# Kernel optimization log

Measured on AMD Instinct MI355X. Metric: run time of the kernel, lower is better.

Reference implementation:

```python
import jax, jax.numpy as jnp
import numpy as np

N, M, D, DV = 16384, 16384, 8, 16
BLOCK = 2048  # row tile size; kernel block is [BLOCK, M], never materialize full [N, M]


def setup_inputs() -> dict:
    key = jax.random.key(0)
    k1, k2, k3, k4 = jax.random.split(key, 4)
    ls = jax.random.uniform(k1, (D,), dtype=jnp.float32)          # per-dim lengthscale weights (positive)
    x = jax.random.normal(k2, (N, D), dtype=jnp.float32)
    y = jax.random.normal(k3, (M, D), dtype=jnp.float32)
    b = jax.random.normal(k4, (M, DV), dtype=jnp.float32)
    return {"ls": ls, "x": x, "y": y, "b": b}


def reference(ls, x, y, b):
    # Matern nu=2.5 kernel-weighted reduction:
    #   d2_ij = sum_d ls_d * (x_id - y_jd)^2
    #   K_ij  = (1 + c1*sqrt(d2) + c2*d2) * exp(-c1*sqrt(d2))   (c1=sqrt(5), c2=sqrt(5/3), as in the torch module)
    #   out_i = sum_j K_ij * b_j   -- computed in row tiles (KeOps-style online reduction)
    c1 = jnp.sqrt(jnp.asarray(5.0, x.dtype))
    c2 = jnp.sqrt(jnp.asarray(5.0 / 3.0, x.dtype))

    def row_block(xi):  # xi: [BLOCK, D]
        diff = xi[:, None, :] - y[None, :, :]                 # [BLOCK, M, D]
        d2 = jnp.einsum('d,bmd->bm', ls, diff * diff)         # [BLOCK, M]
        r = jnp.sqrt(d2)
        k = (1.0 + c1 * r + c2 * d2) * jnp.exp(-c1 * r)       # [BLOCK, M]
        return k @ b                                          # [BLOCK, DV]

    xb = x.reshape(-1, BLOCK, x.shape[1])                     # [N/BLOCK, BLOCK, D]
    out = jax.lax.map(row_block, xb)                          # [N/BLOCK, BLOCK, DV]
    return out.reshape(-1, b.shape[1])                        # [N, DV]
```

## Files before the change

### kernel.cpp

```cpp
#include <hip/hip_runtime.h>
#include <stdint.h>

#define NN 16384
#define MM 16384
#define DD 8
#define DV 16
#define WAVES 4
#define MT 2
#define ROWS_WAVE (MT * 16)
#define ROWS_BLK (WAVES * ROWS_WAVE)
#define JSPLIT 32
#define JCHUNK (MM / JSPLIT)
#define J32 (JCHUNK / 32)

typedef short bf8 __attribute__((ext_vector_type(8)));
typedef short s2v __attribute__((ext_vector_type(2)));
typedef float f32x4 __attribute__((ext_vector_type(4)));

#define C3SQ 10.406844905028037f
#define C2S  (1.2909944487358056f / 10.406844905028037f)
#define LN2  0.6931471805599453f

__device__ __forceinline__ unsigned short f2bf(float f) {
    union { float f; uint32_t u; } c; c.f = f;
    uint32_t u = c.u + 0x7FFF + ((c.u >> 16) & 1);
    return (unsigned short)(u >> 16);
}
__device__ __forceinline__ float bf2f(unsigned short h) {
    union { float f; uint32_t u; } c; c.u = ((uint32_t)h) << 16;
    return c.f;
}

#define BF16_ONE ((short)0x3F80)

__global__ __launch_bounds__(256) void prep_frags(const float* __restrict__ ls,
                                                  const float* __restrict__ y,
                                                  const float* __restrict__ b,
                                                  bf8* __restrict__ ytbl,
                                                  bf8* __restrict__ btbl,
                                                  float4* __restrict__ outz) {
    const int tile = blockIdx.x * 4 + (threadIdx.x >> 6);
    const int lane = threadIdx.x & 63;
    const int n = lane & 15, quad = lane >> 4;

    outz[blockIdx.x * 256 + threadIdx.x] = make_float4(0.f, 0.f, 0.f, 0.f);

    float lsv[DD];
#pragma unroll
    for (int d = 0; d < DD; ++d) lsv[d] = ls[d];

    const float4* yr4 = (const float4*)(y + (size_t)(tile * 16 + n) * DD);
    float4 ya = yr4[0], yb = yr4[1];
    float yv[DD] = {ya.x, ya.y, ya.z, ya.w, yb.x, yb.y, yb.z, yb.w};

    float syv = 0.f;
    unsigned short wh[DD], wl[DD];
#pragma unroll
    for (int d = 0; d < DD; ++d) {
        syv = fmaf(lsv[d] * yv[d], yv[d], syv);
        float w = -2.f * C3SQ * yv[d];
        wh[d] = f2bf(w);
        wl[d] = f2bf(w - bf2f(wh[d]));
    }

    bf8 fr;
    if (quad < 3) {
#pragma unroll
        for (int d = 0; d < DD; ++d)
            fr[d] = (short)((quad == 2) ? wl[d] : wh[d]);
    } else {
        float csy = C3SQ * syv;
        unsigned short sh = f2bf(csy);
        unsigned short sl = f2bf(csy - bf2f(sh));
        fr[0] = (short)sh;
        fr[1] = (short)sl;
        fr[2] = BF16_ONE;
        fr[3] = BF16_ONE;
        fr[4] = 0; fr[5] = 0; fr[6] = 0; fr[7] = 0;
    }
    ytbl[tile * 64 + lane] = fr;

    if (tile < MM / 32) {
        bf8 bfr;
#pragma unroll
        for (int s = 0; s < 8; ++s) {
            int k = quad * 8 + s;
            int jl = (k >> 1) + ((k & 1) << 4);
            float bv = b[(size_t)(tile * 32 + jl) * DV + n];
            bfr[s] = (short)f2bf(bv);
        }
        btbl[tile * 64 + lane] = bfr;
    }
}

__global__ __launch_bounds__(256, 8) void matern_mfma(const float* __restrict__ ls,
                                                      const float* __restrict__ x,
                                                      const bf8* __restrict__ ytbl,
                                                      const bf8* __restrict__ btbl,
                                                      float* __restrict__ out) {
    const int t = threadIdx.x;
    const int lane = t & 63, wave = t >> 6;
    const int n = lane & 15, quad = lane >> 4;
    const int waverow = blockIdx.x * ROWS_BLK + wave * ROWS_WAVE;

    __shared__ __attribute__((aligned(16))) unsigned short klds[WAVES][MT][16][40];

    float lsv[DD];
#pragma unroll
    for (int d = 0; d < DD; ++d) lsv[d] = ls[d];

    bf8 afrag[MT];
#pragma unroll
    for (int mt = 0; mt < MT; ++mt) {
        const float* xr = x + (size_t)(waverow + mt * 16 + n) * DD;
        float sx = 0.f;
        unsigned short xh[DD], xl[DD];
#pragma unroll
        for (int d = 0; d < DD; ++d) {
            float xv = xr[d];
            float xlsv = lsv[d] * xv;
            sx = fmaf(xlsv, xv, sx);
            xh[d] = f2bf(xlsv);
            xl[d] = f2bf(xlsv - bf2f(xh[d]));
        }
        bf8 fr;
        if (quad == 3) {
            float csx = C3SQ * sx;
            unsigned short sh = f2bf(csx);
            unsigned short sl = f2bf(csx - bf2f(sh));
            fr[0] = BF16_ONE;
            fr[1] = BF16_ONE;
            fr[2] = (short)sh;
            fr[3] = (short)sl;
            fr[4] = 0; fr[5] = 0; fr[6] = 0; fr[7] = 0;
        } else {
#pragma unroll
            for (int d = 0; d < DD; ++d)
                fr[d] = (short)((quad == 1) ? xl[d] : xh[d]);
        }
        afrag[mt] = fr;
    }

    f32x4 acc[MT];
#pragma unroll
    for (int mt = 0; mt < MT; ++mt) acc[mt] = (f32x4){0.f, 0.f, 0.f, 0.f};

    const int tile16base = blockIdx.y * (JCHUNK / 16);
    const int tile32base = blockIdx.y * (JCHUNK / 32);

#pragma unroll 1
    for (int it = 0; it < J32; ++it) {
        const int tl0 = tile16base + it * 2;
        bf8 yA = ytbl[(size_t)tl0 * 64 + lane];
        bf8 yB = ytbl[(size_t)(tl0 + 1) * 64 + lane];
        bf8 bb = btbl[(size_t)(tile32base + it) * 64 + lane];

#pragma unroll
        for (int mt = 0; mt < MT; ++mt) {
            f32x4 z = (f32x4){0.f, 0.f, 0.f, 0.f};
            f32x4 s0 = __builtin_amdgcn_mfma_f32_16x16x32_bf16(afrag[mt], yA, z, 0, 0, 0);
            f32x4 s1 = __builtin_amdgcn_mfma_f32_16x16x32_bf16(afrag[mt], yB, z, 0, 0, 0);
#pragma unroll
            for (int s = 0; s < 4; ++s) {
                float a0 = __builtin_fabsf(s0[s]);
                float a1 = __builtin_fabsf(s1[s]);
                float t0 = __builtin_amdgcn_sqrtf(a0);
                float t1 = __builtin_amdgcn_sqrtf(a1);
                float e0 = __builtin_amdgcn_exp2f(-t0);
                float e1 = __builtin_amdgcn_exp2f(-t1);
                float k0 = fmaf(C2S, a0, fmaf(LN2, t0, 1.f)) * e0;
                float k1 = fmaf(C2S, a1, fmaf(LN2, t1, 1.f)) * e1;
                s2v w;
#if __has_builtin(__builtin_amdgcn_cvt_pk_bf16_f32)
                typedef __bf16 bf2v __attribute__((ext_vector_type(2)));
                bf2v pk = __builtin_amdgcn_cvt_pk_bf16_f32(k0, k1);
                union { bf2v v; s2v s; } cv; cv.v = pk;
                w = cv.s;
#else
                w[0] = (short)((__float_as_uint(k0) + 0x8000u) >> 16);
                w[1] = (short)((__float_as_uint(k1) + 0x8000u) >> 16);
#endif
                *(s2v*)&klds[wave][mt][quad * 4 + s][2 * n] = w;
            }
        }
#pragma unroll
        for (int mt = 0; mt < MT; ++mt) {
            const bf8* kp = (const bf8*)&klds[wave][mt][n][quad * 8];
            acc[mt] = __builtin_amdgcn_mfma_f32_16x16x32_bf16(*kp, bb, acc[mt], 0, 0, 0);
        }
    }

#pragma unroll
    for (int mt = 0; mt < MT; ++mt)
#pragma unroll
        for (int s = 0; s < 4; ++s) {
            const int row = waverow + mt * 16 + quad * 4 + s;
            atomicAdd(out + (size_t)row * DV + n, acc[mt][s]);
        }
}

extern "C" void kernel_launch(void* const* d_in, const int* in_sizes, int n_in,
                              void* d_out, int out_size, void* d_ws, size_t ws_size,
                              hipStream_t stream) {
    const float* ls = (const float*)d_in[0];
    const float* x  = (const float*)d_in[1];
    const float* y  = (const float*)d_in[2];
    const float* b  = (const float*)d_in[3];
    float* out = (float*)d_out;

    char* ws = (char*)d_ws;
    bf8* ytbl = (bf8*)ws;
    bf8* btbl = (bf8*)(ws + (1 << 20));

    prep_frags<<<MM / 64, 256, 0, stream>>>(ls, y, b, ytbl, btbl, (float4*)out);
    matern_mfma<<<dim3(NN / ROWS_BLK, JSPLIT), 256, 0, stream>>>(ls, x, ytbl, btbl, out);
}
```

Measured before the change: 136.2 us.

## Prefetch next tile fragments and pack Matern elementwise math into float2 ops

Loads the y and b fragments for the next j-tile one iteration ahead, so global load latency overlaps the current tile's MFMA and transcendental work. Rewrites the per-element kernel evaluation as two-wide float vectors so the compiler can emit packed FMA/mul instructions. Clamps to zero with max instead of fabs, and packs to bf16 with a single perm instead of the cvt builtin. Costs extra registers for the prefetched fragments, which may reduce occupancy. The final iteration issues one redundant wrapped-around load.

```diff
diff --git a/kernel.cpp b/kernel.cpp
--- a/kernel.cpp
+++ b/kernel.cpp
@@ -14,7 +14,7 @@
 #define J32 (JCHUNK / 32)
 
 typedef short bf8 __attribute__((ext_vector_type(8)));
-typedef short s2v __attribute__((ext_vector_type(2)));
+typedef float f32x2 __attribute__((ext_vector_type(2)));
 typedef float f32x4 __attribute__((ext_vector_type(4)));
 
 #define C3SQ 10.406844905028037f
@@ -148,39 +148,42 @@
     const int tile16base = blockIdx.y * (JCHUNK / 16);
     const int tile32base = blockIdx.y * (JCHUNK / 32);
 
+    const bf8* ybase = ytbl + (size_t)tile16base * 64 + lane;
+    const bf8* bbase = btbl + (size_t)tile32base * 64 + lane;
+
+    bf8 yA = ybase[0];
+    bf8 yB = ybase[64];
+    bf8 bb = bbase[0];
+
 #pragma unroll 1
     for (int it = 0; it < J32; ++it) {
-        const int tl0 = tile16base + it * 2;
-        bf8 yA = ytbl[(size_t)tl0 * 64 + lane];
-        bf8 yB = ytbl[(size_t)(tl0 + 1) * 64 + lane];
-        bf8 bb = btbl[(size_t)(tile32base + it) * 64 + lane];
+        const int nx = (it + 1) & (J32 - 1);
+        bf8 pyA = ybase[(size_t)nx * 128];
+        bf8 pyB = ybase[(size_t)nx * 128 + 64];
+        bf8 pbb = bbase[(size_t)nx * 64];
 
 #pragma unroll
         for (int mt = 0; mt < MT; ++mt) {
-            f32x4 z = (f32x4){0.f, 0.f, 0.f, 0.f};
-            f32x4 s0 = __builtin_amdgcn_mfma_f32_16x16x32_bf16(afrag[mt], yA, z, 0, 0, 0);
-            f32x4 s1 = __builtin_amdgcn_mfma_f32_16x16x32_bf16(afrag[mt], yB, z, 0, 0, 0);
+            f32x4 z4 = (f32x4){0.f, 0.f, 0.f, 0.f};
+            f32x4 s0 = __builtin_amdgcn_mfma_f32_16x16x32_bf16(afrag[mt], yA, z4, 0, 0, 0);
+            f32x4 s1 = __builtin_amdgcn_mfma_f32_16x16x32_bf16(afrag[mt], yB, z4, 0, 0, 0);
 #pragma unroll
             for (int s = 0; s < 4; ++s) {
-                float a0 = __builtin_fabsf(s0[s]);
-                float a1 = __builtin_fabsf(s1[s]);
-                float t0 = __builtin_amdgcn_sqrtf(a0);
-                float t1 = __builtin_amdgcn_sqrtf(a1);
-                float e0 = __builtin_amdgcn_exp2f(-t0);
-                float e1 = __builtin_amdgcn_exp2f(-t1);
-                float k0 = fmaf(C2S, a0, fmaf(LN2, t0, 1.f)) * e0;
-                float k1 = fmaf(C2S, a1, fmaf(LN2, t1, 1.f)) * e1;
-                s2v w;
-#if __has_builtin(__builtin_amdgcn_cvt_pk_bf16_f32)
-                typedef __bf16 bf2v __attribute__((ext_vector_type(2)));
-                bf2v pk = __builtin_amdgcn_cvt_pk_bf16_f32(k0, k1);
-                union { bf2v v; s2v s; } cv; cv.v = pk;
-                w = cv.s;
-#else
-                w[0] = (short)((__float_as_uint(k0) + 0x8000u) >> 16);
-                w[1] = (short)((__float_as_uint(k1) + 0x8000u) >> 16);
-#endif
-                *(s2v*)&klds[wave][mt][quad * 4 + s][2 * n] = w;
+                f32x2 a = {s0[s], s1[s]};
+                a = __builtin_elementwise_max(a, (f32x2){0.f, 0.f});
+                f32x2 tt = {__builtin_amdgcn_sqrtf(a[0]),
+                            __builtin_amdgcn_sqrtf(a[1])};
+                f32x2 ee = {__builtin_amdgcn_exp2f(-tt[0]),
+                            __builtin_amdgcn_exp2f(-tt[1])};
+                f32x2 pp = __builtin_elementwise_fma(
+                               (f32x2){C2S, C2S}, a,
+                               __builtin_elementwise_fma((f32x2){LN2, LN2}, tt,
+                                                         (f32x2){1.f, 1.f}));
+                f32x2 kk = pp * ee;
+                unsigned int u0 = __float_as_uint(kk[0]) + 0x8000u;
+                unsigned int u1 = __float_as_uint(kk[1]) + 0x8000u;
+                *(unsigned int*)&klds[wave][mt][quad * 4 + s][2 * n] =
+                    __builtin_amdgcn_perm(u1, u0, 0x07060302u);
             }
         }
 #pragma unroll
@@ -188,6 +191,7 @@
             const bf8* kp = (const bf8*)&klds[wave][mt][n][quad * 8];
             acc[mt] = __builtin_amdgcn_mfma_f32_16x16x32_bf16(*kp, bb, acc[mt], 0, 0, 0);
         }
+        yA = pyA; yB = pyB; bb = pbb;
     }
 
 #pragma unroll
```

After: 144.1 us. 5.8% more time.

## Replace Matern sqrt/exp evaluation with piecewise-linear LDS lookup table

Applied to the files above, without the earlier changes.

Swaps the per-element sqrt and exp2 transcendental evaluation of the Matern kernel for a piecewise-linear approximation. The table is indexed by the float bit pattern, giving log-spaced segments, and each block builds it in LDS before the main loop. This is meant to cut transcendental-unit pressure in the inner loop. In exchange it adds LDS gathers that can hit bank conflicts, a per-block table build plus a barrier, and approximation error on top of the existing bf16 rounding. Values beyond the table range are clamped to zero.

```diff
diff --git a/kernel.cpp b/kernel.cpp
--- a/kernel.cpp
+++ b/kernel.cpp
@@ -21,6 +21,10 @@
 #define C2S  (1.2909944487358056f / 10.406844905028037f)
 #define LN2  0.6931471805599453f
 
+#define KTAB_N 576
+#define KTAB_SHIFT 18
+#define KTAB_OFS 3808
+
 __device__ __forceinline__ unsigned short f2bf(float f) {
     union { float f; uint32_t u; } c; c.f = f;
     uint32_t u = c.u + 0x7FFF + ((c.u >> 16) & 1);
@@ -104,6 +108,22 @@
     const int waverow = blockIdx.x * ROWS_BLK + wave * ROWS_WAVE;
 
     __shared__ __attribute__((aligned(16))) unsigned short klds[WAVES][MT][16][40];
+    __shared__ __attribute__((aligned(16))) float2 ktab[KTAB_N];
+
+    for (int i = t; i < KTAB_N; i += 256) {
+        uint32_t b0 = ((uint32_t)(i + KTAB_OFS)) << KTAB_SHIFT;
+        float z0 = __uint_as_float(b0);
+        float z1 = __uint_as_float(b0 + (1u << KTAB_SHIFT));
+        float t0 = __builtin_amdgcn_sqrtf(z0);
+        float t1 = __builtin_amdgcn_sqrtf(z1);
+        float k0 = fmaf(C2S, z0, fmaf(LN2, t0, 1.f)) * __builtin_amdgcn_exp2f(-t0);
+        float k1 = fmaf(C2S, z1, fmaf(LN2, t1, 1.f)) * __builtin_amdgcn_exp2f(-t1);
+        float S = (k1 - k0) / (z1 - z0);
+        float B = fmaf(-S, z0, k0);
+        if (i == KTAB_N - 1) { S = 0.f; B = 0.f; }
+        ktab[i] = make_float2(B, S);
+    }
+    __syncthreads();
 
     float lsv[DD];
 #pragma unroll
@@ -157,19 +177,21 @@
 
 #pragma unroll
         for (int mt = 0; mt < MT; ++mt) {
-            f32x4 z = (f32x4){0.f, 0.f, 0.f, 0.f};
-            f32x4 s0 = __builtin_amdgcn_mfma_f32_16x16x32_bf16(afrag[mt], yA, z, 0, 0, 0);
-            f32x4 s1 = __builtin_amdgcn_mfma_f32_16x16x32_bf16(afrag[mt], yB, z, 0, 0, 0);
+            f32x4 z4 = (f32x4){0.f, 0.f, 0.f, 0.f};
+            f32x4 s0 = __builtin_amdgcn_mfma_f32_16x16x32_bf16(afrag[mt], yA, z4, 0, 0, 0);
+            f32x4 s1 = __builtin_amdgcn_mfma_f32_16x16x32_bf16(afrag[mt], yB, z4, 0, 0, 0);
 #pragma unroll
             for (int s = 0; s < 4; ++s) {
-                float a0 = __builtin_fabsf(s0[s]);
-                float a1 = __builtin_fabsf(s1[s]);
-                float t0 = __builtin_amdgcn_sqrtf(a0);
-                float t1 = __builtin_amdgcn_sqrtf(a1);
-                float e0 = __builtin_amdgcn_exp2f(-t0);
-                float e1 = __builtin_amdgcn_exp2f(-t1);
-                float k0 = fmaf(C2S, a0, fmaf(LN2, t0, 1.f)) * e0;
-                float k1 = fmaf(C2S, a1, fmaf(LN2, t1, 1.f)) * e1;
+                float z0c = fmaxf(s0[s], 0.f);
+                float z1c = fmaxf(s1[s], 0.f);
+                int i0 = (int)(__float_as_uint(z0c) >> KTAB_SHIFT) - KTAB_OFS;
+                int i1 = (int)(__float_as_uint(z1c) >> KTAB_SHIFT) - KTAB_OFS;
+                i0 = i0 < 0 ? 0 : (i0 > KTAB_N - 1 ? KTAB_N - 1 : i0);
+                i1 = i1 < 0 ? 0 : (i1 > KTAB_N - 1 ? KTAB_N - 1 : i1);
+                float2 e0 = ktab[i0];
+                float2 e1 = ktab[i1];
+                float k0 = fmaf(e0.y, z0c, e0.x);
+                float k1 = fmaf(e1.y, z1c, e1.x);
                 s2v w;
 #if __has_builtin(__builtin_amdgcn_cvt_pk_bf16_f32)
                 typedef __bf16 bf2v __attribute__((ext_vector_type(2)));
```

New measurement: 136.4 us. Within noise of the previous version (+0.2%).

## Compute transposed distance tile to feed MFMA operand directly, dropping LDS round trip

Applied to the files above, without the earlier changes.

Swaps the operand order of the distance MFMA so each lane's output already matches the A-operand layout of the second MFMA. The kernel values are packed straight into registers, which removes the LDS write/read per iteration, and the B-table permutation in prep is changed to match. JSPLIT is also halved, giving fewer, longer j-chunks and fewer atomic adds. The risk is that the new B permutation must exactly match the register layout, and the smaller grid lowers parallelism.

```diff
diff --git a/kernel.cpp b/kernel.cpp
--- a/kernel.cpp
+++ b/kernel.cpp
@@ -9,12 +9,11 @@
 #define MT 2
 #define ROWS_WAVE (MT * 16)
 #define ROWS_BLK (WAVES * ROWS_WAVE)
-#define JSPLIT 32
+#define JSPLIT 16
 #define JCHUNK (MM / JSPLIT)
 #define J32 (JCHUNK / 32)
 
 typedef short bf8 __attribute__((ext_vector_type(8)));
-typedef short s2v __attribute__((ext_vector_type(2)));
 typedef float f32x4 __attribute__((ext_vector_type(4)));
 
 #define C3SQ 10.406844905028037f
@@ -32,6 +31,26 @@
 }
 
 #define BF16_ONE ((short)0x3F80)
+
+__device__ __forceinline__ float ktrans(float z) {
+    float a = __builtin_fabsf(z);
+    float t = __builtin_amdgcn_sqrtf(a);
+    float e = __builtin_amdgcn_exp2f(-t);
+    return fmaf(C2S, a, fmaf(LN2, t, 1.f)) * e;
+}
+
+__device__ __forceinline__ unsigned int pk2(float k0, float k1) {
+#if __has_builtin(__builtin_amdgcn_cvt_pk_bf16_f32)
+    typedef __bf16 bf2v __attribute__((ext_vector_type(2)));
+    union { bf2v v; unsigned int u; } cv;
+    cv.v = __builtin_amdgcn_cvt_pk_bf16_f32(k0, k1);
+    return cv.u;
+#else
+    unsigned int u0 = __float_as_uint(k0) + 0x8000u;
+    unsigned int u1 = __float_as_uint(k1) + 0x8000u;
+    return __builtin_amdgcn_perm(u1, u0, 0x07060302u);
+#endif
+}
 
 __global__ __launch_bounds__(256) void prep_frags(const float* __restrict__ ls,
                                                   const float* __restrict__ y,
@@ -85,7 +104,8 @@
 #pragma unroll
         for (int s = 0; s < 8; ++s) {
             int k = quad * 8 + s;
-            int jl = (k >> 1) + ((k & 1) << 4);
+            int q = k >> 3, r = k & 7;
+            int jl = q * 4 + (r & 3) + ((r & 4) ? 16 : 0);
             float bv = b[(size_t)(tile * 32 + jl) * DV + n];
             bfr[s] = (short)f2bf(bv);
         }
@@ -102,8 +122,6 @@
     const int lane = t & 63, wave = t >> 6;
     const int n = lane & 15, quad = lane >> 4;
     const int waverow = blockIdx.x * ROWS_BLK + wave * ROWS_WAVE;
-
-    __shared__ __attribute__((aligned(16))) unsigned short klds[WAVES][MT][16][40];
 
     float lsv[DD];
 #pragma unroll
@@ -157,36 +175,15 @@
 
 #pragma unroll
         for (int mt = 0; mt < MT; ++mt) {
-            f32x4 z = (f32x4){0.f, 0.f, 0.f, 0.f};
-            f32x4 s0 = __builtin_amdgcn_mfma_f32_16x16x32_bf16(afrag[mt], yA, z, 0, 0, 0);
-            f32x4 s1 = __builtin_amdgcn_mfma_f32_16x16x32_bf16(afrag[mt], yB, z, 0, 0, 0);
-#pragma unroll
-            for (int s = 0; s < 4; ++s) {
-                float a0 = __builtin_fabsf(s0[s]);
-                float a1 = __builtin_fabsf(s1[s]);
-                float t0 = __builtin_amdgcn_sqrtf(a0);
-                float t1 = __builtin_amdgcn_sqrtf(a1);
-                float e0 = __builtin_amdgcn_exp2f(-t0);
-                float e1 = __builtin_amdgcn_exp2f(-t1);
-                float k0 = fmaf(C2S, a0, fmaf(LN2, t0, 1.f)) * e0;
-                float k1 = fmaf(C2S, a1, fmaf(LN2, t1, 1.f)) * e1;
-                s2v w;
-#if __has_builtin(__builtin_amdgcn_cvt_pk_bf16_f32)
-                typedef __bf16 bf2v __attribute__((ext_vector_type(2)));
-                bf2v pk = __builtin_amdgcn_cvt_pk_bf16_f32(k0, k1);
-                union { bf2v v; s2v s; } cv; cv.v = pk;
-                w = cv.s;
-#else
-                w[0] = (short)((__float_as_uint(k0) + 0x8000u) >> 16);
-                w[1] = (short)((__float_as_uint(k1) + 0x8000u) >> 16);
-#endif
-                *(s2v*)&klds[wave][mt][quad * 4 + s][2 * n] = w;
-            }
-        }
-#pragma unroll
-        for (int mt = 0; mt < MT; ++mt) {
-            const bf8* kp = (const bf8*)&klds[wave][mt][n][quad * 8];
-            acc[mt] = __builtin_amdgcn_mfma_f32_16x16x32_bf16(*kp, bb, acc[mt], 0, 0, 0);
+            f32x4 z4 = (f32x4){0.f, 0.f, 0.f, 0.f};
+            f32x4 s0 = __builtin_amdgcn_mfma_f32_16x16x32_bf16(yA, afrag[mt], z4, 0, 0, 0);
+            f32x4 s1 = __builtin_amdgcn_mfma_f32_16x16x32_bf16(yB, afrag[mt], z4, 0, 0, 0);
+            union { bf8 v; unsigned int u[4]; } pa;
+            pa.u[0] = pk2(ktrans(s0[0]), ktrans(s0[1]));
+            pa.u[1] = pk2(ktrans(s0[2]), ktrans(s0[3]));
+            pa.u[2] = pk2(ktrans(s1[0]), ktrans(s1[1]));
+            pa.u[3] = pk2(ktrans(s1[2]), ktrans(s1[3]));
+            acc[mt] = __builtin_amdgcn_mfma_f32_16x16x32_bf16(pa.v, bb, acc[mt], 0, 0, 0);
         }
     }
 
```

After: 135.3 us. About the same (-0.6%).
